# Kernel optimization log

Measured on AMD Instinct MI355X. Metric: run time of the kernel, lower is better.

The kernel has to match this reference:

```python
import jax, jax.numpy as jnp
import numpy as np

SIGMA = 1.0

def setup_inputs() -> dict:
    key = jax.random.key(0)
    k1, k2, k3 = jax.random.split(key, 3)
    X_new = jax.random.normal(k1, (8192, 128), dtype=jnp.float32)
    X_train = jax.random.normal(k2, (32768, 128), dtype=jnp.float32)
    atomic_weights = jax.random.normal(k3, (32768, 1), dtype=jnp.float32)
    return {"X_new": X_new, "X_train": X_train, "atomic_weights": atomic_weights}

def reference(X_new, X_train, atomic_weights):
    x2 = jnp.sum(X_new * X_new, axis=-1, keepdims=True)            # [N_new, 1]
    y2 = jnp.sum(X_train * X_train, axis=-1)                       # [N_train]
    cross = jnp.einsum('nd,md->nm', X_new, X_train)                # [N_new, N_train]
    dist_sq = jnp.maximum(x2 + y2[None, :] - 2.0 * cross, 0.0)
    K_new = jnp.exp(-dist_sq / (2.0 * SIGMA ** 2))
    per_atom_energy = K_new @ atomic_weights                       # [N_new, 1]
    return per_atom_energy
```

## Files before the change

kernel.cpp:

```cpp
#include <hip/hip_runtime.h>
#include <stdint.h>

typedef __attribute__((ext_vector_type(4))) int i32x4;
typedef __attribute__((ext_vector_type(16))) int i32x16;
typedef __attribute__((ext_vector_type(8))) short short8;
typedef __attribute__((ext_vector_type(16))) float f32x16;

#define LOG2E 1.4426950408889634f
#define SA1 22.0f
#define SA1_INV (1.0f / 22.0f)
#define SA2 5500.0f
#define SB1 15.5f
#define SB1_INV (1.0f / 15.5f)
#define SB2 3875.0f
#define K1 (1.0f / (22.0f * 15.5f))
#define K2 (1.0f / 85250.0f)

__device__ inline float fast_exp2(float x) {
#if __has_builtin(__builtin_amdgcn_exp2f)
  return __builtin_amdgcn_exp2f(x);
#else
  float r;
  asm volatile("v_exp_f32 %0, %1" : "=v"(r) : "v"(x));
  return r;
#endif
}

__device__ inline void gload16(const void* g, void* l) {
  __builtin_amdgcn_global_load_lds(
      (const __attribute__((address_space(1))) void*)g,
      (__attribute__((address_space(3))) void*)l, 16, 0, 0);
}
__device__ inline void gload4(const void* g, void* l) {
  __builtin_amdgcn_global_load_lds(
      (const __attribute__((address_space(1))) void*)g,
      (__attribute__((address_space(3))) void*)l, 4, 0, 0);
}

__device__ inline void q4(float4 v, float pre, float s1, float inv_s1,
                          float s2, int& hw, int& lw) {
  float xs[4] = {v.x, v.y, v.z, v.w};
  int h = 0, l = 0;
#pragma unroll
  for (int j = 0; j < 4; ++j) {
    float x = xs[j] * pre;
    float hf = rintf(fminf(fmaxf(x * s1, -127.f), 127.f));
    float rf = x - hf * inv_s1;
    float lf = rintf(fminf(fmaxf(rf * s2, -127.f), 127.f));
    h |= ((int)hf & 255) << (8 * j);
    l |= ((int)lf & 255) << (8 * j);
  }
  hw = h;
  lw = l;
}

__global__ __launch_bounds__(256) void gk_prep(
    const float* __restrict__ Xnew, const float* __restrict__ Xtr,
    const float* __restrict__ w, float* __restrict__ s,
    float* __restrict__ pref, int M, int N) {
  int row = blockIdx.x * 4 + (threadIdx.x >> 6);
  int lane = threadIdx.x & 63;
  if (row >= M + N) return;
  const float* src =
      (row < M) ? (Xtr + (size_t)row * 128) : (Xnew + (size_t)(row - M) * 128);
  float2 v = *(const float2*)(src + lane * 2);
  float ss = v.x * v.x + v.y * v.y;
#pragma unroll
  for (int o = 32; o >= 1; o >>= 1) ss += __shfl_xor(ss, o, 64);
  if (lane == 0) {
    float e = expf(-0.5f * ss);
    if (row < M)
      s[row] = e * w[row];
    else
      pref[row - M] = e;
  }
}

__global__ __launch_bounds__(256) void gk_conv_i8(const float* __restrict__ Xtr,
                                                  char* __restrict__ planes,
                                                  int M) {
  int g = blockIdx.x * 256 + threadIdx.x;
  int row = g >> 3;
  int gr = g & 7;
  if (row >= M) return;
  const float* p = Xtr + (size_t)row * 128 + gr * 16;
  int hw[4], lw[4];
#pragma unroll
  for (int i = 0; i < 4; ++i)
    q4(*(const float4*)(p + i * 4), 1.0f, SA1, SA1_INV, SA2, hw[i], lw[i]);
  int T = row >> 5, r = row & 31;
  size_t base = (size_t)T * 8192 + (gr >> 1) * 1024 + (gr & 1) * 512 + r * 16;
  *(i32x4*)(planes + base) = (i32x4){hw[0], hw[1], hw[2], hw[3]};
  *(i32x4*)(planes + base + 4096) = (i32x4){lw[0], lw[1], lw[2], lw[3]};
}

__global__ __launch_bounds__(256, 3) void gk_main_i8(
    const float* __restrict__ Xnew, const char* __restrict__ planes,
    const float* __restrict__ s, const float* __restrict__ pref,
    float* __restrict__ out, int N, int M, int mchunk) {
  extern __shared__ char dlds[];

  const int t = threadIdx.x;
  const int l = t & 63;
  const int w = t >> 6;
  const int cl = l & 31;
  const int lk = l >> 5;

  const int n0 = blockIdx.x * 256;
  const int M0 = blockIdx.y * mchunk;
  const int Mend = (M0 + mchunk < M) ? (M0 + mchunk) : M;
  const int iters = (Mend - M0) >> 5;
  const int T0 = M0 >> 5;

#define STAGE(tt, buf)                                                      \
  {                                                                         \
    const char* _src = planes + (size_t)(T0 + (tt)) * 8192 + t * 16;        \
    char* _dst = dlds + (buf)*8192 + t * 16;                                \
    gload16(_src, _dst);                                                    \
    gload16(_src + 4096, _dst + 4096);                                      \
    gload4(s + M0 + (tt)*32 + l, dlds + 24576 + (buf)*256);                 \
  }

  STAGE(0, 0);
  if (iters > 1) STAGE(1, 1);

  i32x4 bh[2][4], bl[2][4];
#pragma unroll
  for (int nf = 0; nf < 2; ++nf) {
    const float* pc = Xnew + (size_t)(n0 + w * 64 + nf * 32 + cl) * 128;
#pragma unroll
    for (int kf = 0; kf < 4; ++kf) {
      const float* p = pc + kf * 32 + lk * 16;
      int hw[4], lw[4];
#pragma unroll
      for (int i = 0; i < 4; ++i)
        q4(*(const float4*)(p + i * 4), LOG2E, SB1, SB1_INV, SB2, hw[i], lw[i]);
      bh[nf][kf] = (i32x4){hw[0], hw[1], hw[2], hw[3]};
      bl[nf][kf] = (i32x4){lw[0], lw[1], lw[2], lw[3]};
    }
  }

  float out0 = 0.f, out1 = 0.f;

  asm volatile("s_waitcnt vmcnt(3)" ::: "memory");
  __builtin_amdgcn_s_barrier();

#pragma unroll 1
  for (int it = 0; it < iters; ++it) {
    __builtin_amdgcn_sched_barrier(0);

    if (it + 2 < iters) STAGE(it + 2, (it + 2) % 3);

    const char* buf = dlds + (it % 3) * 8192;
    i32x16 acc_hh0 = {0}, acc_m0 = {0}, acc_hh1 = {0}, acc_m1 = {0};
    __builtin_amdgcn_s_setprio(1);
#pragma unroll
    for (int kf = 0; kf < 4; ++kf) {
      const char* kb = buf + kf * 1024 + lk * 512 + cl * 16;
      i32x4 ah = *(const i32x4*)(kb);
      i32x4 al = *(const i32x4*)(kb + 4096);
      acc_hh0 = __builtin_amdgcn_mfma_i32_32x32x32_i8(ah, bh[0][kf], acc_hh0, 0, 0, 0);
      acc_hh1 = __builtin_amdgcn_mfma_i32_32x32x32_i8(ah, bh[1][kf], acc_hh1, 0, 0, 0);
      acc_m0 = __builtin_amdgcn_mfma_i32_32x32x32_i8(ah, bl[0][kf], acc_m0, 0, 0, 0);
      acc_m1 = __builtin_amdgcn_mfma_i32_32x32x32_i8(ah, bl[1][kf], acc_m1, 0, 0, 0);
      acc_m0 = __builtin_amdgcn_mfma_i32_32x32x32_i8(al, bh[0][kf], acc_m0, 0, 0, 0);
      acc_m1 = __builtin_amdgcn_mfma_i32_32x32x32_i8(al, bh[1][kf], acc_m1, 0, 0, 0);
    }
    __builtin_amdgcn_s_setprio(0);

    const float4* sl4 = (const float4*)(dlds + 24576 + (it % 3) * 256);
#pragma unroll
    for (int q = 0; q < 4; ++q) {
      float4 sv = sl4[q * 2 + lk];
#pragma unroll
      for (int j = 0; j < 4; ++j) {
        int r = q * 4 + j;
        float svj = (&sv.x)[j];
        float c0 = (float)acc_hh0[r] * K1 + (float)acc_m0[r] * K2;
        float c1 = (float)acc_hh1[r] * K1 + (float)acc_m1[r] * K2;
        out0 += fast_exp2(c0) * svj;
        out1 += fast_exp2(c1) * svj;
      }
    }

    if (it + 1 < iters) {
      if (it + 2 < iters) {
        asm volatile("s_waitcnt vmcnt(3)" ::: "memory");
      } else {
        asm volatile("s_waitcnt vmcnt(0)" ::: "memory");
      }
      __builtin_amdgcn_s_barrier();
    }
  }

  out0 += __shfl_xor(out0, 32, 64);
  out1 += __shfl_xor(out1, 32, 64);
  if (l < 32) {
    int n = n0 + w * 64 + l;
    atomicAdd(out + n, pref[n] * out0);
    n += 32;
    atomicAdd(out + n, pref[n] * out1);
  }
#undef STAGE
}

__device__ inline unsigned swz_fb(unsigned off) {
  return off ^ (((off >> 8) & 7u) << 4);
}
__device__ inline void split8(float x0, float x1, float x2, float x3,
                              float x4, float x5, float x6, float x7,
                              float scale, short8& hi, short8& lo) {
  float xs[8] = {x0, x1, x2, x3, x4, x5, x6, x7};
#pragma unroll
  for (int i = 0; i < 8; ++i) {
    float v = xs[i] * scale;
    unsigned u = __float_as_uint(v);
    float hf = __uint_as_float(u & 0xffff0000u);
    float rr = v - hf;
    hi[i] = (short)(u >> 16);
    lo[i] = (short)(__float_as_uint(rr) >> 16);
  }
}

__global__ __launch_bounds__(256, 2) void gk_main_fb(
    const float* __restrict__ Xnew, const float* __restrict__ Xtr,
    const float* __restrict__ s, const float* __restrict__ pref,
    float* __restrict__ out, int N, int M, int mchunk) {
  __shared__ __attribute__((aligned(16))) char lds[33024];
  const int t = threadIdx.x;
  const int l = t & 63;
  const int w = t >> 6;
  const int lrow = l & 31;
  const int lk = l >> 5;
  const int n0 = blockIdx.x * 256;
  const int M0 = blockIdx.y * mchunk;
  const int iters = mchunk >> 6;

  short8 bh[2][8], bl[2][8];
  {
    const int colbase = n0 + w * 64;
#pragma unroll
    for (int nf = 0; nf < 2; ++nf) {
      int col = colbase + nf * 32 + lrow;
      const float* p = Xnew + (size_t)col * 128 + lk * 8;
#pragma unroll
      for (int kf = 0; kf < 8; ++kf) {
        float4 f0 = *(const float4*)(p + kf * 16);
        float4 f1 = *(const float4*)(p + kf * 16 + 4);
        split8(f0.x, f0.y, f0.z, f0.w, f1.x, f1.y, f1.z, f1.w, LOG2E,
               bh[nf][kf], bl[nf][kf]);
      }
    }
  }

  float out0 = 0.f, out1 = 0.f;
  float4 ga[4][2];
  float sreg = 0.f;
  {
    const float* abase = Xtr + (size_t)M0 * 128;
#pragma unroll
    for (int j = 0; j < 4; ++j) {
      int c = t + j * 256;
      int row = c >> 4, oct = c & 15;
      const float* p = abase + (size_t)row * 128 + oct * 8;
      ga[j][0] = *(const float4*)p;
      ga[j][1] = *(const float4*)(p + 4);
    }
    if (t < 64) sreg = s[M0 + t];
  }

#pragma unroll 1
  for (int it = 0; it < iters; ++it) {
    __syncthreads();
#pragma unroll
    for (int j = 0; j < 4; ++j) {
      int c = t + j * 256;
      int row = c >> 4, oct = c & 15;
      unsigned off = swz_fb((unsigned)(row * 256 + oct * 16));
      short8 hi, lo;
      split8(ga[j][0].x, ga[j][0].y, ga[j][0].z, ga[j][0].w, ga[j][1].x,
             ga[j][1].y, ga[j][1].z, ga[j][1].w, 1.0f, hi, lo);
      *(short8*)(lds + off) = hi;
      *(short8*)(lds + 16384 + off) = lo;
    }
    if (t < 64) *(float*)(lds + 32768 + t * 4) = sreg;
    __syncthreads();
    if (it + 1 < iters) {
      const float* abase = Xtr + (size_t)(M0 + (it + 1) * 64) * 128;
#pragma unroll
      for (int j = 0; j < 4; ++j) {
        int c = t + j * 256;
        int row = c >> 4, oct = c & 15;
        const float* p = abase + (size_t)row * 128 + oct * 8;
        ga[j][0] = *(const float4*)p;
        ga[j][1] = *(const float4*)(p + 4);
      }
      if (t < 64) sreg = s[M0 + (it + 1) * 64 + t];
    }
#pragma unroll
    for (int mf = 0; mf < 2; ++mf) {
      f32x16 acc0 = {0, 0, 0, 0, 0, 0, 0, 0, 0, 0, 0, 0, 0, 0, 0, 0};
      f32x16 acc1 = {0, 0, 0, 0, 0, 0, 0, 0, 0, 0, 0, 0, 0, 0, 0, 0};
#pragma unroll
      for (int kf = 0; kf < 8; ++kf) {
        unsigned off =
            swz_fb((unsigned)((mf * 32 + lrow) * 256 + kf * 32 + lk * 16));
        short8 ah = *(const short8*)(lds + off);
        short8 al = *(const short8*)(lds + 16384 + off);
        acc0 = __builtin_amdgcn_mfma_f32_32x32x16_bf16(ah, bh[0][kf], acc0, 0, 0, 0);
        acc1 = __builtin_amdgcn_mfma_f32_32x32x16_bf16(ah, bh[1][kf], acc1, 0, 0, 0);
        acc0 = __builtin_amdgcn_mfma_f32_32x32x16_bf16(ah, bl[0][kf], acc0, 0, 0, 0);
        acc1 = __builtin_amdgcn_mfma_f32_32x32x16_bf16(ah, bl[1][kf], acc1, 0, 0, 0);
        acc0 = __builtin_amdgcn_mfma_f32_32x32x16_bf16(al, bh[0][kf], acc0, 0, 0, 0);
        acc1 = __builtin_amdgcn_mfma_f32_32x32x16_bf16(al, bh[1][kf], acc1, 0, 0, 0);
      }
      const float* sl = (const float*)(lds + 32768 + mf * 128);
#pragma unroll
      for (int r = 0; r < 16; ++r) {
        int row = (r & 3) + 8 * (r >> 2) + 4 * lk;
        float sv = sl[row];
        out0 += fast_exp2(acc0[r]) * sv;
        out1 += fast_exp2(acc1[r]) * sv;
      }
    }
  }
  out0 += __shfl_xor(out0, 32, 64);
  out1 += __shfl_xor(out1, 32, 64);
  if (l < 32) {
    int n = n0 + w * 64 + l;
    atomicAdd(out + n, pref[n] * out0);
    n += 32;
    atomicAdd(out + n, pref[n] * out1);
  }
}

extern "C" void kernel_launch(void* const* d_in, const int* in_sizes, int n_in,
                              void* d_out, int out_size, void* d_ws,
                              size_t ws_size, hipStream_t stream) {
  const float* Xnew = (const float*)d_in[0];
  const float* Xtr = (const float*)d_in[1];
  const float* wts = (const float*)d_in[2];
  float* out = (float*)d_out;

  const int N = in_sizes[0] / 128;
  const int M = in_sizes[1] / 128;

  char* ws = (char*)d_ws;
  float* s_ws = (float*)ws;
  float* pref_ws = s_ws + M;
  char* planes_ws = ws + (size_t)(M + N) * 4;
  const size_t need = (size_t)(M + N) * 4 + (size_t)M * 256;

  hipMemsetAsync(d_out, 0, (size_t)N * sizeof(float), stream);

  int rows = M + N;
  gk_prep<<<dim3((rows + 3) / 4), 256, 0, stream>>>(Xnew, Xtr, wts, s_ws,
                                                    pref_ws, M, N);

  if (ws_size >= need) {
    gk_conv_i8<<<dim3(M * 8 / 256), 256, 0, stream>>>(Xtr, planes_ws, M);
    const int SPLIT = 24;
    const int CH = ((M + SPLIT - 1) / SPLIT + 31) & ~31;
    dim3 grid(N / 256, SPLIT);
    gk_main_i8<<<grid, 256, 25344, stream>>>(Xnew, planes_ws, s_ws, pref_ws,
                                             out, N, M, CH);
  } else {
    const int SPLIT = 16;
    dim3 grid(N / 256, SPLIT);
    gk_main_fb<<<grid, 256, 0, stream>>>(Xnew, Xtr, s_ws, pref_ws, out, N, M,
                                         M / SPLIT);
  }
}
```

Before: 142.7 us.

## Use 512-thread blocks with one column fragment per wave and power-of-two int8 split scales

Blocks grow to 512 threads (8 waves), each wave covering 32 columns instead of 64, so per-wave MFMA work and register use drop while more waves hide latency. Both operands now share power-of-two split scales (16 and 4096), so the high and cross accumulators combine with a shift-add and one scale before the exp2. The staging loads use all 512 threads with one 16-byte load each, the M split goes from 24 to 16, and the tail-chunk bound handling is removed. The trade-offs are reduced reuse of the A tile per wave, changed quantisation precision, and reliance on M dividing evenly into 16 chunks of 32-row tiles.

```diff
diff --git a/kernel.cpp b/kernel.cpp
--- a/kernel.cpp
+++ b/kernel.cpp
@@ -7,14 +7,10 @@
 typedef __attribute__((ext_vector_type(16))) float f32x16;
 
 #define LOG2E 1.4426950408889634f
-#define SA1 22.0f
-#define SA1_INV (1.0f / 22.0f)
-#define SA2 5500.0f
-#define SB1 15.5f
-#define SB1_INV (1.0f / 15.5f)
-#define SB2 3875.0f
-#define K1 (1.0f / (22.0f * 15.5f))
-#define K2 (1.0f / 85250.0f)
+#define S1 16.0f
+#define S1_INV 0.0625f
+#define S2 4096.0f
+#define K2 (1.0f / 65536.0f)
 
 __device__ inline float fast_exp2(float x) {
 #if __has_builtin(__builtin_amdgcn_exp2f)
@@ -37,16 +33,15 @@
       (__attribute__((address_space(3))) void*)l, 4, 0, 0);
 }
 
-__device__ inline void q4(float4 v, float pre, float s1, float inv_s1,
-                          float s2, int& hw, int& lw) {
+__device__ inline void q4(float4 v, float pre, int& hw, int& lw) {
   float xs[4] = {v.x, v.y, v.z, v.w};
   int h = 0, l = 0;
 #pragma unroll
   for (int j = 0; j < 4; ++j) {
     float x = xs[j] * pre;
-    float hf = rintf(fminf(fmaxf(x * s1, -127.f), 127.f));
-    float rf = x - hf * inv_s1;
-    float lf = rintf(fminf(fmaxf(rf * s2, -127.f), 127.f));
+    float hf = rintf(fminf(fmaxf(x * S1, -127.f), 127.f));
+    float rf = x - hf * S1_INV;
+    float lf = rintf(fminf(fmaxf(rf * S2, -127.f), 127.f));
     h |= ((int)hf & 255) << (8 * j);
     l |= ((int)lf & 255) << (8 * j);
   }
@@ -87,14 +82,14 @@
   int hw[4], lw[4];
 #pragma unroll
   for (int i = 0; i < 4; ++i)
-    q4(*(const float4*)(p + i * 4), 1.0f, SA1, SA1_INV, SA2, hw[i], lw[i]);
+    q4(*(const float4*)(p + i * 4), 1.0f, hw[i], lw[i]);
   int T = row >> 5, r = row & 31;
   size_t base = (size_t)T * 8192 + (gr >> 1) * 1024 + (gr & 1) * 512 + r * 16;
   *(i32x4*)(planes + base) = (i32x4){hw[0], hw[1], hw[2], hw[3]};
   *(i32x4*)(planes + base + 4096) = (i32x4){lw[0], lw[1], lw[2], lw[3]};
 }
 
-__global__ __launch_bounds__(256, 3) void gk_main_i8(
+__global__ __launch_bounds__(512, 4) void gk_main_i8(
     const float* __restrict__ Xnew, const char* __restrict__ planes,
     const float* __restrict__ s, const float* __restrict__ pref,
     float* __restrict__ out, int N, int M, int mchunk) {
@@ -108,41 +103,41 @@
 
   const int n0 = blockIdx.x * 256;
   const int M0 = blockIdx.y * mchunk;
-  const int Mend = (M0 + mchunk < M) ? (M0 + mchunk) : M;
-  const int iters = (Mend - M0) >> 5;
+  const int iters = mchunk >> 5;
   const int T0 = M0 >> 5;
 
-#define STAGE(tt, buf)                                                      \
-  {                                                                         \
-    const char* _src = planes + (size_t)(T0 + (tt)) * 8192 + t * 16;        \
-    char* _dst = dlds + (buf)*8192 + t * 16;                                \
-    gload16(_src, _dst);                                                    \
-    gload16(_src + 4096, _dst + 4096);                                      \
-    gload4(s + M0 + (tt)*32 + l, dlds + 24576 + (buf)*256);                 \
+#define STAGE(tt, buf)                                                 \
+  {                                                                    \
+    gload16(planes + (size_t)(T0 + (tt)) * 8192 + t * 16,              \
+            dlds + (buf)*8192 + t * 16);                               \
+    gload4(s + M0 + (tt)*32 + l, dlds + 24576 + (buf)*256);            \
   }
 
   STAGE(0, 0);
   if (iters > 1) STAGE(1, 1);
 
-  i32x4 bh[2][4], bl[2][4];
-#pragma unroll
-  for (int nf = 0; nf < 2; ++nf) {
-    const float* pc = Xnew + (size_t)(n0 + w * 64 + nf * 32 + cl) * 128;
+  i32x4 bh[4], bl[4];
+  {
+    const float* pc = Xnew + (size_t)(n0 + w * 32 + cl) * 128;
 #pragma unroll
     for (int kf = 0; kf < 4; ++kf) {
       const float* p = pc + kf * 32 + lk * 16;
       int hw[4], lw[4];
 #pragma unroll
       for (int i = 0; i < 4; ++i)
-        q4(*(const float4*)(p + i * 4), LOG2E, SB1, SB1_INV, SB2, hw[i], lw[i]);
-      bh[nf][kf] = (i32x4){hw[0], hw[1], hw[2], hw[3]};
-      bl[nf][kf] = (i32x4){lw[0], lw[1], lw[2], lw[3]};
-    }
-  }
-
-  float out0 = 0.f, out1 = 0.f;
-
-  asm volatile("s_waitcnt vmcnt(3)" ::: "memory");
+        q4(*(const float4*)(p + i * 4), LOG2E, hw[i], lw[i]);
+      bh[kf] = (i32x4){hw[0], hw[1], hw[2], hw[3]};
+      bl[kf] = (i32x4){lw[0], lw[1], lw[2], lw[3]};
+    }
+  }
+
+  float out0 = 0.f;
+
+  if (iters > 1) {
+    asm volatile("s_waitcnt vmcnt(2)" ::: "memory");
+  } else {
+    asm volatile("s_waitcnt vmcnt(0)" ::: "memory");
+  }
   __builtin_amdgcn_s_barrier();
 
 #pragma unroll 1
@@ -152,19 +147,16 @@
     if (it + 2 < iters) STAGE(it + 2, (it + 2) % 3);
 
     const char* buf = dlds + (it % 3) * 8192;
-    i32x16 acc_hh0 = {0}, acc_m0 = {0}, acc_hh1 = {0}, acc_m1 = {0};
+    i32x16 acc_hh = {0}, acc_m = {0};
     __builtin_amdgcn_s_setprio(1);
 #pragma unroll
     for (int kf = 0; kf < 4; ++kf) {
       const char* kb = buf + kf * 1024 + lk * 512 + cl * 16;
       i32x4 ah = *(const i32x4*)(kb);
       i32x4 al = *(const i32x4*)(kb + 4096);
-      acc_hh0 = __builtin_amdgcn_mfma_i32_32x32x32_i8(ah, bh[0][kf], acc_hh0, 0, 0, 0);
-      acc_hh1 = __builtin_amdgcn_mfma_i32_32x32x32_i8(ah, bh[1][kf], acc_hh1, 0, 0, 0);
-      acc_m0 = __builtin_amdgcn_mfma_i32_32x32x32_i8(ah, bl[0][kf], acc_m0, 0, 0, 0);
-      acc_m1 = __builtin_amdgcn_mfma_i32_32x32x32_i8(ah, bl[1][kf], acc_m1, 0, 0, 0);
-      acc_m0 = __builtin_amdgcn_mfma_i32_32x32x32_i8(al, bh[0][kf], acc_m0, 0, 0, 0);
-      acc_m1 = __builtin_amdgcn_mfma_i32_32x32x32_i8(al, bh[1][kf], acc_m1, 0, 0, 0);
+      acc_hh = __builtin_amdgcn_mfma_i32_32x32x32_i8(ah, bh[kf], acc_hh, 0, 0, 0);
+      acc_m = __builtin_amdgcn_mfma_i32_32x32x32_i8(ah, bl[kf], acc_m, 0, 0, 0);
+      acc_m = __builtin_amdgcn_mfma_i32_32x32x32_i8(al, bh[kf], acc_m, 0, 0, 0);
     }
     __builtin_amdgcn_s_setprio(0);
 
@@ -175,17 +167,14 @@
 #pragma unroll
       for (int j = 0; j < 4; ++j) {
         int r = q * 4 + j;
-        float svj = (&sv.x)[j];
-        float c0 = (float)acc_hh0[r] * K1 + (float)acc_m0[r] * K2;
-        float c1 = (float)acc_hh1[r] * K1 + (float)acc_m1[r] * K2;
-        out0 += fast_exp2(c0) * svj;
-        out1 += fast_exp2(c1) * svj;
+        float c = (float)((acc_hh[r] << 8) + acc_m[r]) * K2;
+        out0 += fast_exp2(c) * (&sv.x)[j];
       }
     }
 
     if (it + 1 < iters) {
       if (it + 2 < iters) {
-        asm volatile("s_waitcnt vmcnt(3)" ::: "memory");
+        asm volatile("s_waitcnt vmcnt(2)" ::: "memory");
       } else {
         asm volatile("s_waitcnt vmcnt(0)" ::: "memory");
       }
@@ -194,12 +183,9 @@
   }
 
   out0 += __shfl_xor(out0, 32, 64);
-  out1 += __shfl_xor(out1, 32, 64);
   if (l < 32) {
-    int n = n0 + w * 64 + l;
+    int n = n0 + w * 32 + l;
     atomicAdd(out + n, pref[n] * out0);
-    n += 32;
-    atomicAdd(out + n, pref[n] * out1);
   }
 #undef STAGE
 }
@@ -359,11 +345,10 @@
 
   if (ws_size >= need) {
     gk_conv_i8<<<dim3(M * 8 / 256), 256, 0, stream>>>(Xtr, planes_ws, M);
-    const int SPLIT = 24;
-    const int CH = ((M + SPLIT - 1) / SPLIT + 31) & ~31;
+    const int SPLIT = 16;
     dim3 grid(N / 256, SPLIT);
-    gk_main_i8<<<grid, 256, 25344, stream>>>(Xnew, planes_ws, s_ws, pref_ws,
-                                             out, N, M, CH);
+    gk_main_i8<<<grid, 512, 25344, stream>>>(Xnew, planes_ws, s_ws, pref_ws,
+                                             out, N, M, M / SPLIT);
   } else {
     const int SPLIT = 16;
     dim3 grid(N / 256, SPLIT);
```

Result: faster. 131.2 us (-8.0%).
